# Optimization experiments

Hardware: AMD Instinct MI355X
Metric: run time of the kernel (lower is better)

## Reference

```python
import jax, jax.numpy as jnp
import numpy as np
from jax import lax

DIM = 128
K = 3
PAD = K // 2


def setup_inputs() -> dict:
    key = jax.random.key(0)
    k1, k2, k3, k4, k5 = jax.random.split(key, 5)
    B, H, W = 64, 32, 32
    wdim = DIM * DIM * K * K + DIM  # 147584
    # scale question_rep (it encodes conv weights) for numerical sanity
    question_rep = jax.random.normal(k1, (B, wdim), dtype=jnp.float32) * 0.05
    lhs_rep = jax.random.normal(k2, (B, DIM, H, W), dtype=jnp.float32)
    rhs_rep = jax.random.normal(k3, (B, DIM, H, W), dtype=jnp.float32)
    proj_w = jax.random.normal(k4, (DIM, 2 * DIM), dtype=jnp.float32) * (1.0 / np.sqrt(2 * DIM))
    proj_b = jax.random.normal(k5, (DIM,), dtype=jnp.float32) * 0.01
    return {"question_rep": question_rep, "lhs_rep": lhs_rep,
            "rhs_rep": rhs_rep, "proj_w": proj_w, "proj_b": proj_b}


def _per_sample_conv(x, w, b):
    # x: [dim, H, W], w: [dim, dim, K, K], b: [dim]
    y = lax.conv_general_dilated(
        x[None], w, window_strides=(1, 1),
        padding=[(PAD, PAD), (PAD, PAD)],
        dimension_numbers=("NCHW", "OIHW", "NCHW"))
    return y[0] + b[:, None, None]


def reference(question_rep, lhs_rep, rhs_rep, proj_w, proj_b):
    B = question_rep.shape[0]
    wdim = DIM * DIM * K * K
    cnn_weight = question_rep[:, :wdim].reshape(B, DIM, DIM, K, K)
    cnn_bias = question_rep[:, wdim:]  # [B, dim]
    # 1x1 projection conv: cat along channels then contract
    cat = jnp.concatenate([lhs_rep, rhs_rep], axis=1)  # [B, 2*dim, H, W]
    cnn_inp = jnp.einsum("bchw,oc->bohw", cat, proj_w) + proj_b[None, :, None, None]
    # per-sample dynamic conv, vectorized over batch (equiv. grouped conv)
    out = jax.vmap(_per_sample_conv)(cnn_inp, cnn_weight, cnn_bias)
    return out
```

## Files before the change

kernel.cpp:

```cpp
#include <hip/hip_runtime.h>
#include <hip/hip_bf16.h>

#define QSTRIDE 147584
#define WOFF    147456

typedef __attribute__((ext_vector_type(8))) short bf16x8;
typedef __attribute__((ext_vector_type(4))) float f32x4;

static __device__ __forceinline__ ushort f2bf(float f) {
  union { float f; unsigned u; } x; x.f = f;
  unsigned r = x.u + 0x7fffu + ((x.u >> 16) & 1u);
  return (ushort)(r >> 16);
}
static __device__ __forceinline__ unsigned pk2(ushort a, ushort b) {
  return (unsigned)a | ((unsigned)b << 16);
}

__global__ __launch_bounds__(256) void pack_w_kernel(const float* __restrict__ q,
                                                     ushort* __restrict__ wt2) {
  __shared__ float Ls[4608];
  int b = blockIdx.x >> 3, ogrp = blockIdx.x & 7;
  int t = threadIdx.x;
  const float* gbase = q + (size_t)b * QSTRIDE + (size_t)ogrp * 16 * 1152;
  ushort* dstb = wt2 + (size_t)b * 147456;
  int o_loc = t >> 6;
  int ci    = (t & 63) * 2;
  int cq    = ci >> 5, coff = ci & 31;
  for (int r = 0; r < 4; ++r) {
    __syncthreads();
    const float* gs = gbase + r * 4608;
#pragma unroll
    for (int i = 0; i < 18; ++i) Ls[i * 256 + t] = gs[i * 256 + t];
    __syncthreads();
    int o_full = ogrp * 16 + r * 4 + o_loc;
    const float* v = Ls + o_loc * 1152 + ci * 9;
    float a[18];
#pragma unroll
    for (int i = 0; i < 18; ++i) a[i] = v[i];
    ushort* dd = dstb + (size_t)cq * 4096 + o_full * 32 + coff;
#pragma unroll
    for (int tap = 0; tap < 9; ++tap) {
      unsigned pkv = pk2(f2bf(a[tap]), f2bf(a[9 + tap]));
      *(unsigned*)(dd + (size_t)tap * 16384) = pkv;
    }
  }
}

__global__ __launch_bounds__(256) void pack_pw_kernel(const float* __restrict__ pw,
                                                      ushort* __restrict__ pwb2) {
  int tg = blockIdx.x * 256 + threadIdx.x;
  int o  = tg >> 5;
  int c0 = (tg & 31) * 8;
  const float4* s4 = (const float4*)(pw + (size_t)o * 256 + c0);
  float4 f0 = s4[0], f1 = s4[1];
  uint4 pkv;
  pkv.x = pk2(f2bf(f0.x), f2bf(f0.y)); pkv.y = pk2(f2bf(f0.z), f2bf(f0.w));
  pkv.z = pk2(f2bf(f1.x), f2bf(f1.y)); pkv.w = pk2(f2bf(f1.z), f2bf(f1.w));
  *(uint4*)(pwb2 + (size_t)(c0 >> 5) * 4096 + o * 32 + (c0 & 31)) = pkv;
}

__global__ __launch_bounds__(256, 2) void fused_conv_kernel(const ushort* __restrict__ wt2,
                                                            const ushort* __restrict__ pwb2,
                                                            const float* __restrict__ lhs,
                                                            const float* __restrict__ rhs,
                                                            const float* __restrict__ pb,
                                                            const float* __restrict__ q,
                                                            float* __restrict__ out) {
  __shared__ ushort Bs[4][6][34][32];
  int blk = blockIdx.x;
  int b = blk & 63, tile = blk >> 6;
  int p0 = tile * 128, h0 = tile * 4;
  int t = threadIdx.x;
  int lane = t & 63, wv = t >> 6;
  int quad = lane >> 4, li = lane & 15;

  if (t < 48) {
    int cq = t & 3, side = (t >> 2) & 1, rr = t >> 3;
    uint4* z4 = (uint4*)&Bs[cq][rr][side ? 33 : 0][0];
    uint4 z; z.x = z.y = z.z = z.w = 0u;
    z4[0] = z; z4[1] = z; z4[2] = z; z4[3] = z;
  }

  {
    int rk[3], wk[3], hk[3]; bool lv[3];
#pragma unroll
    for (int k = 0; k < 3; ++k) {
      int nt = wv * 3 + k;
      rk[k] = nt >> 1;
      wk[k] = (nt & 1) * 16;
      hk[k] = h0 - 1 + rk[k];
      lv[k] = (hk[k] >= 0) && (hk[k] < 32);
    }
    f32x4 acc[3][8] = {};
#pragma unroll
    for (int c = 0; c < 8; ++c) {
      const float* basep = (c < 4 ? lhs : rhs) + (size_t)b * 131072
                         + (size_t)((c & 3) * 32 + quad * 8) * 1024;
      bf16x8 bg[3];
#pragma unroll
      for (int k = 0; k < 3; ++k) {
        union { uint4 u; bf16x8 v; } bu;
        if (lv[k]) {
          const float* s = basep + hk[k] * 32 + wk[k] + li;
          float f[8];
#pragma unroll
          for (int j = 0; j < 8; ++j) f[j] = s[(size_t)j * 1024];
          bu.u.x = pk2(f2bf(f[0]), f2bf(f[1]));
          bu.u.y = pk2(f2bf(f[2]), f2bf(f[3]));
          bu.u.z = pk2(f2bf(f[4]), f2bf(f[5]));
          bu.u.w = pk2(f2bf(f[6]), f2bf(f[7]));
        } else {
          bu.u.x = bu.u.y = bu.u.z = bu.u.w = 0u;
        }
        bg[k] = bu.v;
      }
      const ushort* ap = pwb2 + (size_t)c * 4096 + li * 32 + quad * 8;
#pragma unroll
      for (int mi = 0; mi < 8; ++mi) {
        bf16x8 af = *(const bf16x8*)(ap + mi * 512);
#pragma unroll
        for (int k = 0; k < 3; ++k)
          acc[k][mi] = __builtin_amdgcn_mfma_f32_16x16x32_bf16(af, bg[k], acc[k][mi], 0, 0, 0);
      }
    }
#pragma unroll
    for (int k = 0; k < 3; ++k) {
#pragma unroll
      for (int mi = 0; mi < 8; ++mi) {
        int o0 = mi * 16 + quad * 4;
        uint2 pkv;
        if (lv[k]) {
          float4 bias = *(const float4*)(pb + o0);
          f32x4 a = acc[k][mi];
          pkv.x = pk2(f2bf(a.x + bias.x), f2bf(a.y + bias.y));
          pkv.y = pk2(f2bf(a.z + bias.z), f2bf(a.w + bias.w));
        } else {
          pkv.x = 0u; pkv.y = 0u;
        }
        *(uint2*)&Bs[o0 >> 5][rk[k]][wk[k] + li + 1][o0 & 31] = pkv;
      }
    }
  }
  __syncthreads();

  int m0 = (wv & 1) * 64, n0 = (wv >> 1) * 64;
  f32x4 acc2[4][4] = {};
  const ushort* wtb = wt2 + (size_t)b * 147456;
#pragma unroll
  for (int cq = 0; cq < 4; ++cq) {
    const ushort* wcq = wtb + (size_t)cq * 4096;
#pragma unroll
    for (int tap = 0; tap < 9; ++tap) {
      const ushort* ar = wcq + (size_t)tap * 16384;
      int kh = tap / 3, kw = tap - kh * 3;
      bf16x8 af[4], bg[4];
#pragma unroll
      for (int mi = 0; mi < 4; ++mi)
        af[mi] = *(const bf16x8*)(ar + (m0 + mi*16 + li) * 32 + quad * 8);
#pragma unroll
      for (int ni = 0; ni < 4; ++ni) {
        int pl = n0 + ni*16 + li;
        int hh = pl >> 5, ww = pl & 31;
        bg[ni] = *(const bf16x8*)&Bs[cq][hh + kh][ww + kw][quad * 8];
      }
#pragma unroll
      for (int mi = 0; mi < 4; ++mi)
#pragma unroll
        for (int ni = 0; ni < 4; ++ni)
          acc2[mi][ni] = __builtin_amdgcn_mfma_f32_16x16x32_bf16(af[mi], bg[ni], acc2[mi][ni], 0, 0, 0);
    }
  }

  const float* qb = q + (size_t)b * QSTRIDE + WOFF;
  float* ob = out + (size_t)b * 128 * 1024 + p0;
#pragma unroll
  for (int mi = 0; mi < 4; ++mi) {
    int o0 = m0 + mi*16 + quad*4;
    float4 bias = *(const float4*)(qb + o0);
#pragma unroll
    for (int ni = 0; ni < 4; ++ni) {
      int pl = n0 + ni*16 + li;
      float* dp = ob + (size_t)o0 * 1024 + pl;
      f32x4 a = acc2[mi][ni];
      dp[0]    = a.x + bias.x;
      dp[1024] = a.y + bias.y;
      dp[2048] = a.z + bias.z;
      dp[3072] = a.w + bias.w;
    }
  }
}

extern "C" void kernel_launch(void* const* d_in, const int* in_sizes, int n_in,
                              void* d_out, int out_size, void* d_ws, size_t ws_size,
                              hipStream_t stream) {
  const float* q   = (const float*)d_in[0];
  const float* lhs = (const float*)d_in[1];
  const float* rhs = (const float*)d_in[2];
  const float* pw  = (const float*)d_in[3];
  const float* pb  = (const float*)d_in[4];
  float* out = (float*)d_out;

  char* ws = (char*)d_ws;
  ushort* wt2  = (ushort*)(ws);
  ushort* pwb2 = (ushort*)(ws + 18874368);

  pack_w_kernel    <<<512, 256, 0, stream>>>(q, wt2);
  pack_pw_kernel   <<<16,  256, 0, stream>>>(pw, pwb2);
  fused_conv_kernel<<<512, 256, 0, stream>>>(wt2, pwb2, lhs, rhs, pb, q, out);
}
```

Baseline: 181.4 us.

## Pre-transpose inputs to bf16 channel-minor layout and stage weight packing in LDS

Adds a transpose kernel that converts the lhs/rhs activations to bf16 in a pixel-major layout with 32 contiguous channels per pixel. The fused conv can then load each MFMA B fragment with a single 16-byte load instead of eight strided scalar float loads plus conversions. The weight pack kernel now assembles its output in shared memory and writes it out with coalesced 16-byte stores instead of scattered 4-byte stores. The cost is an extra kernel launch and an extra round trip of the activations through memory in bf16.

After: 186.8 us. +2.9%, slower.

```diff
diff --git a/kernel.cpp b/kernel.cpp
--- a/kernel.cpp
+++ b/kernel.cpp
@@ -18,11 +18,11 @@
 
 __global__ __launch_bounds__(256) void pack_w_kernel(const float* __restrict__ q,
                                                      ushort* __restrict__ wt2) {
-  __shared__ float Ls[4608];
+  __shared__ float  Ls[4608];
+  __shared__ ushort Lw[9 * 4 * 16 * 32];
   int b = blockIdx.x >> 3, ogrp = blockIdx.x & 7;
   int t = threadIdx.x;
   const float* gbase = q + (size_t)b * QSTRIDE + (size_t)ogrp * 16 * 1152;
-  ushort* dstb = wt2 + (size_t)b * 147456;
   int o_loc = t >> 6;
   int ci    = (t & 63) * 2;
   int cq    = ci >> 5, coff = ci & 31;
@@ -32,17 +32,24 @@
 #pragma unroll
     for (int i = 0; i < 18; ++i) Ls[i * 256 + t] = gs[i * 256 + t];
     __syncthreads();
-    int o_full = ogrp * 16 + r * 4 + o_loc;
+    int o_in = r * 4 + o_loc;
     const float* v = Ls + o_loc * 1152 + ci * 9;
     float a[18];
 #pragma unroll
     for (int i = 0; i < 18; ++i) a[i] = v[i];
-    ushort* dd = dstb + (size_t)cq * 4096 + o_full * 32 + coff;
 #pragma unroll
     for (int tap = 0; tap < 9; ++tap) {
       unsigned pkv = pk2(f2bf(a[tap]), f2bf(a[9 + tap]));
-      *(unsigned*)(dd + (size_t)tap * 16384) = pkv;
-    }
+      *(unsigned*)&Lw[((tap * 4 + cq) * 16 + o_in) * 32 + coff] = pkv;
+    }
+  }
+  __syncthreads();
+  int wv = t >> 6, l = t & 63;
+  ushort* dstb = wt2 + (size_t)b * 147456 + (size_t)ogrp * 16 * 32;
+#pragma unroll
+  for (int tap = 0; tap < 9; ++tap) {
+    const uint4 val = *(const uint4*)&Lw[(tap * 4 + wv) * 512 + l * 8];
+    *(uint4*)(dstb + (size_t)(tap * 4 + wv) * 4096 + l * 8) = val;
   }
 }
 
@@ -59,10 +66,42 @@
   *(uint4*)(pwb2 + (size_t)(c0 >> 5) * 4096 + o * 32 + (c0 & 31)) = pkv;
 }
 
+__global__ __launch_bounds__(256) void transpose_x_kernel(const float* __restrict__ lhs,
+                                                          const float* __restrict__ rhs,
+                                                          ushort* __restrict__ xt) {
+  __shared__ ushort Ts[32][132];
+  int b = blockIdx.y;
+  int c = blockIdx.x & 7, half = blockIdx.x >> 3;
+  const float* src = (c < 4 ? lhs : rhs) + (size_t)b * 131072 + (size_t)(c & 3) * 32768;
+  ushort* dst = xt + (size_t)(b * 8 + c) * 32768;
+  int t = threadIdx.x;
+  int chw = t >> 3, pxg = (t & 7) * 16;
+  int pxr = t >> 1, chr = (t & 1) * 16;
+#pragma unroll
+  for (int pt = 0; pt < 4; ++pt) {
+    int p0 = half * 512 + pt * 128;
+    if (pt) __syncthreads();
+    const float* s = src + (size_t)chw * 1024 + p0 + pxg;
+#pragma unroll
+    for (int i = 0; i < 4; ++i) {
+      float4 f = *(const float4*)(s + 4 * i);
+      uint2 pk;
+      pk.x = pk2(f2bf(f.x), f2bf(f.y));
+      pk.y = pk2(f2bf(f.z), f2bf(f.w));
+      *(uint2*)&Ts[chw][pxg + 4 * i] = pk;
+    }
+    __syncthreads();
+    ushort g[16];
+#pragma unroll
+    for (int j = 0; j < 16; ++j) g[j] = Ts[chr + j][pxr];
+    *(uint4*)(dst + (size_t)(p0 + pxr) * 32 + chr)     = *(uint4*)&g[0];
+    *(uint4*)(dst + (size_t)(p0 + pxr) * 32 + chr + 8) = *(uint4*)&g[8];
+  }
+}
+
 __global__ __launch_bounds__(256, 2) void fused_conv_kernel(const ushort* __restrict__ wt2,
                                                             const ushort* __restrict__ pwb2,
-                                                            const float* __restrict__ lhs,
-                                                            const float* __restrict__ rhs,
+                                                            const ushort* __restrict__ xt,
                                                             const float* __restrict__ pb,
                                                             const float* __restrict__ q,
                                                             float* __restrict__ out) {
@@ -91,24 +130,17 @@
       hk[k] = h0 - 1 + rk[k];
       lv[k] = (hk[k] >= 0) && (hk[k] < 32);
     }
+    const ushort* xtb = xt + (size_t)b * 8 * 32768;
     f32x4 acc[3][8] = {};
 #pragma unroll
     for (int c = 0; c < 8; ++c) {
-      const float* basep = (c < 4 ? lhs : rhs) + (size_t)b * 131072
-                         + (size_t)((c & 3) * 32 + quad * 8) * 1024;
       bf16x8 bg[3];
 #pragma unroll
       for (int k = 0; k < 3; ++k) {
         union { uint4 u; bf16x8 v; } bu;
         if (lv[k]) {
-          const float* s = basep + hk[k] * 32 + wk[k] + li;
-          float f[8];
-#pragma unroll
-          for (int j = 0; j < 8; ++j) f[j] = s[(size_t)j * 1024];
-          bu.u.x = pk2(f2bf(f[0]), f2bf(f[1]));
-          bu.u.y = pk2(f2bf(f[2]), f2bf(f[3]));
-          bu.u.z = pk2(f2bf(f[4]), f2bf(f[5]));
-          bu.u.w = pk2(f2bf(f[6]), f2bf(f[7]));
+          int px = hk[k] * 32 + wk[k] + li;
+          bu.u = *(const uint4*)(xtb + ((size_t)c * 1024 + px) * 32 + quad * 8);
         } else {
           bu.u.x = bu.u.y = bu.u.z = bu.u.w = 0u;
         }
@@ -203,8 +235,10 @@
   char* ws = (char*)d_ws;
   ushort* wt2  = (ushort*)(ws);
   ushort* pwb2 = (ushort*)(ws + 18874368);
-
-  pack_w_kernel    <<<512, 256, 0, stream>>>(q, wt2);
-  pack_pw_kernel   <<<16,  256, 0, stream>>>(pw, pwb2);
-  fused_conv_kernel<<<512, 256, 0, stream>>>(wt2, pwb2, lhs, rhs, pb, q, out);
-}
+  ushort* xt   = (ushort*)(ws + 18939904);
+
+  pack_w_kernel     <<<512, 256, 0, stream>>>(q, wt2);
+  pack_pw_kernel    <<<16,  256, 0, stream>>>(pw, pwb2);
+  transpose_x_kernel<<<dim3(16, 64), 256, 0, stream>>>(lhs, rhs, xt);
+  fused_conv_kernel <<<512, 256, 0, stream>>>(wt2, pwb2, xt, pb, q, out);
+}
```
